# Kernel optimization log

Hardware: AMD Instinct MI355X
Metric: run time of the kernel (lower is better)

Reference implementation:

```python
import jax, jax.numpy as jnp
import numpy as np

IN, H, OUT, FC_H = 8, 128, 4, 64
BN_EPS = 1e-5


def _lstm_cell(x, h, c, Wih, Whh, bih, bhh):
    # PyTorch gate order: i, f, g, o
    z = x @ Wih.T + h @ Whh.T + (bih + bhh)  # [B, 4H]
    i, f, g, o = jnp.split(z, 4, axis=-1)
    i, f, o = jax.nn.sigmoid(i), jax.nn.sigmoid(f), jax.nn.sigmoid(o)
    g = jnp.tanh(g)
    c = f * c + i * g
    h = o * jnp.tanh(c)
    return h, c


def setup_inputs() -> dict:
    key = jax.random.key(0)
    ks = jax.random.split(key, 20)
    s = 0.05
    inp = {
        "x": jax.random.normal(ks[0], (4096, 512, IN), jnp.float32),
        # LSTM layer 0 (input_size -> H)
        "Wih0": jax.random.normal(ks[1], (4 * H, IN), jnp.float32) * s,
        "Whh0": jax.random.normal(ks[2], (4 * H, H), jnp.float32) * s,
        "bih0": jax.random.normal(ks[3], (4 * H,), jnp.float32) * s,
        "bhh0": jax.random.normal(ks[4], (4 * H,), jnp.float32) * s,
        # LSTM layer 1 (H -> H)
        "Wih1": jax.random.normal(ks[5], (4 * H, H), jnp.float32) * s,
        "Whh1": jax.random.normal(ks[6], (4 * H, H), jnp.float32) * s,
        "bih1": jax.random.normal(ks[7], (4 * H,), jnp.float32) * s,
        "bhh1": jax.random.normal(ks[8], (4 * H,), jnp.float32) * s,
        # BatchNorm1d(H) in eval mode: affine params + running stats
        "bn_gamma": jnp.ones((H,), jnp.float32),
        "bn_beta": jnp.zeros((H,), jnp.float32),
        "bn_mean": jax.random.normal(ks[9], (H,), jnp.float32) * s,
        "bn_var": jax.random.uniform(ks[10], (H,), jnp.float32, 0.5, 1.5),
        # fc: Linear(H, 64) -> ReLU -> Linear(64, OUT)
        "W1": jax.random.normal(ks[11], (FC_H, H), jnp.float32) * s,
        "b1": jax.random.normal(ks[12], (FC_H,), jnp.float32) * s,
        "W2": jax.random.normal(ks[13], (OUT, FC_H), jnp.float32) * s,
        "b2": jax.random.normal(ks[14], (OUT,), jnp.float32) * s,
        # feedback: Linear(OUT, IN)
        "Wf": jax.random.normal(ks[15], (IN, OUT), jnp.float32) * s,
        "bf": jax.random.normal(ks[16], (IN,), jnp.float32) * s,
        "prediction_steps": 64,
    }
    return inp


def reference(x, Wih0, Whh0, bih0, bhh0, Wih1, Whh1, bih1, bhh1,
              bn_gamma, bn_beta, bn_mean, bn_var, W1, b1, W2, b2, Wf, bf,
              prediction_steps):
    B = x.shape[0]
    h0 = jnp.zeros((B, H), x.dtype)
    state0 = (h0, h0, h0, h0)  # (h_l0, c_l0, h_l1, c_l1)

    def step(state, xt):
        hl0, cl0, hl1, cl1 = state
        hl0, cl0 = _lstm_cell(xt, hl0, cl0, Wih0, Whh0, bih0, bhh0)
        hl1, cl1 = _lstm_cell(hl0, hl1, cl1, Wih1, Whh1, bih1, bhh1)
        return (hl0, cl0, hl1, cl1), None

    # Encoding pass over the full sequence (seq_len=1 per step in torch loop)
    xs = jnp.swapaxes(x, 0, 1)  # [T, B, IN]
    state, _ = jax.lax.scan(step, state0, xs)

    def fc(h):
        hn = (h - bn_mean) * jax.lax.rsqrt(bn_var + BN_EPS) * bn_gamma + bn_beta
        return jax.nn.relu(hn @ W1.T + b1) @ W2.T + b2

    def dec_step(carry, _):
        hl0, cl0, hl1, cl1, xin = carry
        hl0, cl0 = _lstm_cell(xin, hl0, cl0, Wih0, Whh0, bih0, bhh0)
        hl1, cl1 = _lstm_cell(hl0, hl1, cl1, Wih1, Whh1, bih1, bhh1)
        out = fc(hl1)                 # [B, OUT]
        xin = out @ Wf.T + bf         # feedback -> next input [B, IN]
        return (hl0, cl0, hl1, cl1, xin), out

    carry0 = (*state, x[:, -1, :])
    _, outs = jax.lax.scan(dec_step, carry0, None, length=prediction_steps)
    return jnp.swapaxes(outs, 0, 1)  # [B, prediction_steps, OUT]
```

## Files before the change

### kernel.cpp

```cpp
#include <hip/hip_runtime.h>

#define THREADS 512
#define BT 16
#define TLEN 512
#define HD 128
#define NT 4
#define WSTR 132
#define HSTR 136

#define SC_IFO (-1.4426950408889634f)
#define SC_G   ( 2.8853900817779268f)

typedef __attribute__((ext_vector_type(8))) short bf16x8;
typedef __attribute__((ext_vector_type(4))) float f32x4;

__device__ __forceinline__ short f2bf(float f) {
  unsigned u = __float_as_uint(f);
  u += 0x7fff + ((u >> 16) & 1);
  return (short)(u >> 16);
}

__device__ __forceinline__ unsigned cvt_pk_bf16(float lo, float hi) {
  unsigned r;
  asm("v_cvt_pk_bf16_f32 %0, %1, %2" : "=v"(r) : "v"(lo), "v"(hi));
  return r;
}

__device__ __forceinline__ bf16x8 pack8(f32x4 a, f32x4 b) {
  bf16x8 r;
  r[0]=f2bf(a[0]); r[1]=f2bf(a[1]); r[2]=f2bf(a[2]); r[3]=f2bf(a[3]);
  r[4]=f2bf(b[0]); r[5]=f2bf(b[1]); r[6]=f2bf(b[2]); r[7]=f2bf(b[3]);
  return r;
}
__device__ __forceinline__ bf16x8 load8(const float* p) {
  const f32x4* q4 = (const f32x4*)p;
  return pack8(q4[0], q4[1]);
}
__device__ __forceinline__ bf16x8 load8s(const float* p, float s) {
  const f32x4* q4 = (const f32x4*)p;
  return pack8(q4[0] * s, q4[1] * s);
}

__global__ __launch_bounds__(THREADS, 2) void lstm_kernel(
    const float* __restrict__ xg,
    const float* __restrict__ Wih0, const float* __restrict__ Whh0,
    const float* __restrict__ bih0, const float* __restrict__ bhh0,
    const float* __restrict__ Wih1, const float* __restrict__ Whh1,
    const float* __restrict__ bih1, const float* __restrict__ bhh1,
    const float* __restrict__ gma, const float* __restrict__ bta,
    const float* __restrict__ mu,  const float* __restrict__ var,
    const float* __restrict__ W1,  const float* __restrict__ b1,
    const float* __restrict__ W2,  const float* __restrict__ b2,
    const float* __restrict__ Wf,  const float* __restrict__ bfv,
    const int* __restrict__ psP,
    float* __restrict__ dout)
{
  __shared__ __align__(16) short WhhL[512*WSTR];
  __shared__ __align__(16) short h0A[2][BT*HSTR];
  __shared__ __align__(16) short h1A[2][BT*HSTR];
  __shared__ __align__(16) short xA[2][BT*32];
  __shared__ float a1L[64*BT];
  __shared__ float W2L[4*65];
  __shared__ float outL[4*BT];
  __shared__ float WfL[8*4];
  __shared__ float b2L[4];
  __shared__ float bfL[8];
  __shared__ float b1cL[64];
  __shared__ float sLs[HD];

  const int tid = threadIdx.x;
  const int w   = tid >> 6;
  const int l   = tid & 63;
  const int ln  = l & 15;
  const int q   = l >> 4;
  const int gb0 = blockIdx.x * BT;
  const int ps  = psP[0];

  for (int i = tid; i < BT*32; i += THREADS) { xA[0][i] = 0; xA[1][i] = 0; }
  for (int i = tid; i < BT*HSTR; i += THREADS) {
    h0A[0][i] = 0; h0A[1][i] = 0; h1A[0][i] = 0; h1A[1][i] = 0;
  }
  if (tid < BT) {
    xA[0][tid*32 + 8] = (short)0x3F80;
    xA[1][tid*32 + 8] = (short)0x3F80;
  }
  if (tid < HD) sLs[tid] = gma[tid] * rsqrtf(var[tid] + 1e-5f);
  if (tid < 260) { int o = tid / 65, p = tid % 65; W2L[tid] = (p < 64) ? W2[o*64 + p] : 0.f; }
  if (tid < 32) WfL[tid] = Wf[tid];
  if (tid < 4)  b2L[tid] = b2[tid];
  if (tid < 8)  bfL[tid] = bfv[tid];
  for (int i = tid; i < 512*HD; i += THREADS) {
    int og = i >> 7, k = i & 127;
    float sc = ((og >> 7) == 2) ? SC_G : SC_IFO;
    WhhL[og*WSTR + k] = f2bf(Whh0[i] * sc);
  }

  bf16x8 wih0f[NT], wih1f[NT][4], whh1f[NT][4];
  float b1sum[NT];
  #pragma unroll
  for (int nt = 0; nt < NT; nt++) {
    int og = nt*HD + (w << 4) + ln;
    const float sc = (nt == 2) ? SC_G : SC_IFO;
    {
      bf16x8 r;
      #pragma unroll
      for (int j = 0; j < 8; j++) {
        int k = q*8 + j;
        float v = 0.f;
        if (k < 8) v = Wih0[og*8 + k];
        else if (k == 8) v = bih0[og] + bhh0[og];
        r[j] = f2bf(v * sc);
      }
      wih0f[nt] = r;
    }
    #pragma unroll
    for (int kk = 0; kk < 4; kk++) {
      int k0 = kk*32 + q*8;
      wih1f[nt][kk] = load8s(Wih1 + og*HD + k0, sc);
      whh1f[nt][kk] = load8s(Whh1 + og*HD + k0, sc);
    }
    b1sum[nt] = (bih1[og] + bhh1[og]) * sc;
  }
  __syncthreads();

  if (tid < 64) {
    float acc = b1[tid];
    for (int j = 0; j < HD; j++)
      acc += (bta[j] - mu[j]*sLs[j]) * W1[tid*HD + j];
    b1cL[tid] = acc;
  }
  if (tid < 128) {
    const int b = tid >> 3, i2 = tid & 7;
    xA[0][b*32 + i2] = f2bf(xg[(size_t)(gb0 + b)*(TLEN*8) + i2]);
  }
  __syncthreads();

  f32x4 c0s = {0.f,0.f,0.f,0.f};
  f32x4 c1s = {0.f,0.f,0.f,0.f};

  const int aoffX = ln*32   + q*8;
  const int aoffH = ln*HSTR + q*8;
  const int hwoff = (q*4)*HSTR + (w<<4) + ln;

  auto gates = [&](const f32x4& gi, const f32x4& gf, const f32x4& gg, const f32x4& go,
                   f32x4& cs, short* hw) {
    float hv[4];
    #pragma unroll
    for (int r = 0; r < 4; r++) {
      float ei = __builtin_amdgcn_exp2f(gi[r]);
      float ef = __builtin_amdgcn_exp2f(gf[r]);
      float eg = __builtin_amdgcn_exp2f(gg[r]);
      float eo = __builtin_amdgcn_exp2f(go[r]);
      float f   = __builtin_amdgcn_rcpf(1.0f + ef);
      float rig = __builtin_amdgcn_rcpf((1.0f + ei) * (1.0f + eg));
      float igs = (SC_G * eg - SC_G) * rig;
      float c   = f * cs[r] + igs;
      cs[r] = c;
      float ec  = __builtin_amdgcn_exp2f(c);
      float roc = __builtin_amdgcn_rcpf((1.0f + eo) * (1.0f + ec));
      hv[r] = (ec - 1.0f) * roc;
    }
    unsigned p01 = cvt_pk_bf16(hv[0], hv[1]);
    unsigned p23 = cvt_pk_bf16(hv[2], hv[3]);
    hw[0*HSTR] = (short)p01;
    hw[1*HSTR] = (short)(p01 >> 16);
    hw[2*HSTR] = (short)p23;
    hw[3*HSTR] = (short)(p23 >> 16);
  };

  auto layer0 = [&](const short* xr, const bf16x8* ah, short* h0w) {
    bf16x8 ax = *(const bf16x8*)(xr + aoffX);
    f32x4 ac[NT];
    #pragma unroll
    for (int nt = 0; nt < NT; nt++) {
      const int cb = (nt*HD + (w<<4) + ln)*WSTR + q*8;
      f32x4 a = {0.f,0.f,0.f,0.f};
      a = __builtin_amdgcn_mfma_f32_16x16x32_bf16(ax, wih0f[nt], a, 0, 0, 0);
      #pragma unroll
      for (int kk = 0; kk < 4; kk++) {
        bf16x8 wb = *(const bf16x8*)(WhhL + cb + kk*32);
        a = __builtin_amdgcn_mfma_f32_16x16x32_bf16(ah[kk], wb, a, 0, 0, 0);
      }
      ac[nt] = a;
    }
    gates(ac[0], ac[1], ac[2], ac[3], c0s, h0w + hwoff);
  };

  auto layer1 = [&](const bf16x8* ah, const short* h1r, short* h1w) {
    bf16x8 a1k[4];
    #pragma unroll
    for (int kk = 0; kk < 4; kk++)
      a1k[kk] = *(const bf16x8*)(h1r + aoffH + kk*32);
    f32x4 ac[NT];
    #pragma unroll
    for (int nt = 0; nt < NT; nt++) {
      f32x4 a; a[0]=a[1]=a[2]=a[3]=b1sum[nt];
      #pragma unroll
      for (int kk = 0; kk < 4; kk++) {
        a = __builtin_amdgcn_mfma_f32_16x16x32_bf16(ah[kk],  wih1f[nt][kk], a, 0, 0, 0);
        a = __builtin_amdgcn_mfma_f32_16x16x32_bf16(a1k[kk], whh1f[nt][kk], a, 0, 0, 0);
      }
      ac[nt] = a;
    }
    gates(ac[0], ac[1], ac[2], ac[3], c1s, h1w + hwoff);
  };

  auto enc_iter = [&](int k, const short* xr, short* xw,
                      const short* h0r, short* h0w,
                      const short* h1r, short* h1w, bool doL0, bool doL1) {
    const int b = tid >> 3, i2 = tid & 7;
    const bool pf = doL0 && (k + 1 < TLEN) && (tid < 128);
    float xp = 0.f;
    if (pf) xp = xg[(size_t)(gb0 + b)*(TLEN*8) + (size_t)(k+1)*8 + i2];
    bf16x8 ah[4];
    #pragma unroll
    for (int kk = 0; kk < 4; kk++)
      ah[kk] = *(const bf16x8*)(h0r + aoffH + kk*32);
    if (doL0) layer0(xr, ah, h0w);
    if (doL1) layer1(ah, h1r, h1w);
    if (pf) xw[b*32 + i2] = f2bf(xp);
    __syncthreads();
  };

  enc_iter(0, xA[0], xA[1], h0A[1], h0A[0], h1A[0], h1A[1], true, false);
  enc_iter(1, xA[1], xA[0], h0A[0], h0A[1], h1A[1], h1A[0], true, true);
  for (int k = 2; k < TLEN; k += 2) {
    enc_iter(k,     xA[0], xA[1], h0A[1], h0A[0], h1A[0], h1A[1], true, true);
    enc_iter(k + 1, xA[1], xA[0], h0A[0], h0A[1], h1A[1], h1A[0], true, true);
  }
  enc_iter(TLEN, xA[0], xA[1], h0A[1], h0A[0], h1A[0], h1A[1], false, true);

  bf16x8 w1f[4];
  #pragma unroll
  for (int kk = 0; kk < 4; kk++) {
    bf16x8 r;
    if (w < 4) {
      int p = w*16 + ln;
      #pragma unroll
      for (int j = 0; j < 8; j++) {
        int k = kk*32 + q*8 + j;
        r[j] = f2bf(sLs[k] * W1[p*HD + k]);
      }
    } else {
      #pragma unroll
      for (int j = 0; j < 8; j++) r[j] = 0;
    }
    w1f[kk] = r;
  }

  for (int s = 0; s < ps; s++) {
    int rb = (s & 1) ^ 1;
    __syncthreads();
    {
      bf16x8 ah[4];
      #pragma unroll
      for (int kk = 0; kk < 4; kk++)
        ah[kk] = *(const bf16x8*)(h0A[rb] + aoffH + kk*32);
      layer0(xA[1], ah, h0A[rb^1]);
    }
    __syncthreads();
    {
      bf16x8 ah[4];
      #pragma unroll
      for (int kk = 0; kk < 4; kk++)
        ah[kk] = *(const bf16x8*)(h0A[rb^1] + aoffH + kk*32);
      layer1(ah, h1A[rb], h1A[rb^1]);
    }
    const short* h1n = h1A[rb^1];
    __syncthreads();
    if (w < 4) {
      f32x4 aa = {0.f,0.f,0.f,0.f};
      #pragma unroll
      for (int kk = 0; kk < 4; kk++) {
        bf16x8 ahn = *(const bf16x8*)(h1n + aoffH + kk*32);
        aa = __builtin_amdgcn_mfma_f32_16x16x32_bf16(ahn, w1f[kk], aa, 0, 0, 0);
      }
      float bb = b1cL[w*16 + ln];
      #pragma unroll
      for (int r = 0; r < 4; r++)
        a1L[(w*16 + ln)*16 + q*4 + r] = fmaxf(aa[r] + bb, 0.f);
    }
    __syncthreads();
    if (tid < 64) {
      int b = tid & 15, o = tid >> 4;
      float acc2 = b2L[o];
      for (int p = 0; p < 64; p++)
        acc2 += a1L[p*16 + b] * W2L[o*65 + p];
      dout[(size_t)(gb0 + b)*(ps*4) + s*4 + o] = acc2;
      outL[o*16 + b] = acc2;
    }
    __syncthreads();
    if (tid < 128) {
      int b = tid >> 3, i2 = tid & 7;
      float v = bfL[i2];
      #pragma unroll
      for (int o = 0; o < 4; o++) v += outL[o*16 + b] * WfL[i2*4 + o];
      xA[1][b*32 + i2] = f2bf(v);
    }
  }
}

extern "C" void kernel_launch(void* const* d_in, const int* in_sizes, int n_in,
                              void* d_out, int out_size, void* d_ws, size_t ws_size,
                              hipStream_t stream) {
  (void)in_sizes; (void)n_in; (void)d_ws; (void)ws_size; (void)out_size;
  lstm_kernel<<<dim3(4096/BT), dim3(THREADS), 0, stream>>>(
      (const float*)d_in[0],  (const float*)d_in[1],  (const float*)d_in[2],
      (const float*)d_in[3],  (const float*)d_in[4],  (const float*)d_in[5],
      (const float*)d_in[6],  (const float*)d_in[7],  (const float*)d_in[8],
      (const float*)d_in[9],  (const float*)d_in[10], (const float*)d_in[11],
      (const float*)d_in[12], (const float*)d_in[13], (const float*)d_in[14],
      (const float*)d_in[15], (const float*)d_in[16], (const float*)d_in[17],
      (const float*)d_in[18], (const int*)d_in[19],   (float*)d_out);
}
```

Measured before the change: 1.401 ms.

## Fold feedback into FC2 weights and interleave layer MFMA chains in encoder

Precomputes a combined Wf·W2 matrix and bias so the decoder's next input comes straight from the ReLU activations. This removes one barrier and the serial outL→feedback stage, and the feedback and output dot products now run in parallel on separate thread groups. The encoder step is also inlined so both layers' MFMA chains are issued before either gate computation, which should increase instruction-level overlap. The cost is higher register pressure from holding both accumulators and the h1 operands at once.

```diff
diff --git a/kernel.cpp b/kernel.cpp
--- a/kernel.cpp
+++ b/kernel.cpp
@@ -31,10 +31,6 @@
   r[0]=f2bf(a[0]); r[1]=f2bf(a[1]); r[2]=f2bf(a[2]); r[3]=f2bf(a[3]);
   r[4]=f2bf(b[0]); r[5]=f2bf(b[1]); r[6]=f2bf(b[2]); r[7]=f2bf(b[3]);
   return r;
-}
-__device__ __forceinline__ bf16x8 load8(const float* p) {
-  const f32x4* q4 = (const f32x4*)p;
-  return pack8(q4[0], q4[1]);
 }
 __device__ __forceinline__ bf16x8 load8s(const float* p, float s) {
   const f32x4* q4 = (const f32x4*)p;
@@ -61,10 +57,9 @@
   __shared__ __align__(16) short xA[2][BT*32];
   __shared__ float a1L[64*BT];
   __shared__ float W2L[4*65];
-  __shared__ float outL[4*BT];
-  __shared__ float WfL[8*4];
+  __shared__ float WcL[8*68];
+  __shared__ float bcL[8];
   __shared__ float b2L[4];
-  __shared__ float bfL[8];
   __shared__ float b1cL[64];
   __shared__ float sLs[HD];
 
@@ -86,9 +81,20 @@
   }
   if (tid < HD) sLs[tid] = gma[tid] * rsqrtf(var[tid] + 1e-5f);
   if (tid < 260) { int o = tid / 65, p = tid % 65; W2L[tid] = (p < 64) ? W2[o*64 + p] : 0.f; }
-  if (tid < 32) WfL[tid] = Wf[tid];
+  {
+    int i0 = tid >> 6, p = tid & 63;
+    float acc = 0.f;
+    #pragma unroll
+    for (int o = 0; o < 4; o++) acc += Wf[i0*4 + o] * W2[o*64 + p];
+    WcL[i0*68 + p] = acc;
+  }
+  if (tid < 8) {
+    float acc = bfv[tid];
+    #pragma unroll
+    for (int o = 0; o < 4; o++) acc += Wf[tid*4 + o] * b2[o];
+    bcL[tid] = acc;
+  }
   if (tid < 4)  b2L[tid] = b2[tid];
-  if (tid < 8)  bfL[tid] = bfv[tid];
   for (int i = tid; i < 512*HD; i += THREADS) {
     int og = i >> 7, k = i & 127;
     float sc = ((og >> 7) == 2) ? SC_G : SC_IFO;
@@ -216,8 +222,42 @@
     #pragma unroll
     for (int kk = 0; kk < 4; kk++)
       ah[kk] = *(const bf16x8*)(h0r + aoffH + kk*32);
-    if (doL0) layer0(xr, ah, h0w);
-    if (doL1) layer1(ah, h1r, h1w);
+    bf16x8 a1k[4];
+    if (doL1) {
+      #pragma unroll
+      for (int kk = 0; kk < 4; kk++)
+        a1k[kk] = *(const bf16x8*)(h1r + aoffH + kk*32);
+    }
+    f32x4 ac0[NT], ac1[NT];
+    if (doL0) {
+      bf16x8 ax = *(const bf16x8*)(xr + aoffX);
+      #pragma unroll
+      for (int nt = 0; nt < NT; nt++) {
+        const int cb = (nt*HD + (w<<4) + ln)*WSTR + q*8;
+        f32x4 a = {0.f,0.f,0.f,0.f};
+        a = __builtin_amdgcn_mfma_f32_16x16x32_bf16(ax, wih0f[nt], a, 0, 0, 0);
+        #pragma unroll
+        for (int kk = 0; kk < 4; kk++) {
+          bf16x8 wb = *(const bf16x8*)(WhhL + cb + kk*32);
+          a = __builtin_amdgcn_mfma_f32_16x16x32_bf16(ah[kk], wb, a, 0, 0, 0);
+        }
+        ac0[nt] = a;
+      }
+    }
+    if (doL1) {
+      #pragma unroll
+      for (int nt = 0; nt < NT; nt++) {
+        f32x4 a; a[0]=a[1]=a[2]=a[3]=b1sum[nt];
+        #pragma unroll
+        for (int kk = 0; kk < 4; kk++) {
+          a = __builtin_amdgcn_mfma_f32_16x16x32_bf16(ah[kk],  wih1f[nt][kk], a, 0, 0, 0);
+          a = __builtin_amdgcn_mfma_f32_16x16x32_bf16(a1k[kk], whh1f[nt][kk], a, 0, 0, 0);
+        }
+        ac1[nt] = a;
+      }
+    }
+    if (doL0) gates(ac0[0], ac0[1], ac0[2], ac0[3], c0s, h0w + hwoff);
+    if (doL1) gates(ac1[0], ac1[1], ac1[2], ac1[3], c1s, h1w + hwoff);
     if (pf) xw[b*32 + i2] = f2bf(xp);
     __syncthreads();
   };
@@ -281,21 +321,18 @@
         a1L[(w*16 + ln)*16 + q*4 + r] = fmaxf(aa[r] + bb, 0.f);
     }
     __syncthreads();
-    if (tid < 64) {
-      int b = tid & 15, o = tid >> 4;
+    if (tid < 128) {
+      int b = tid >> 3, i2 = tid & 7;
+      float v = bcL[i2];
+      for (int p = 0; p < 64; p++)
+        v += a1L[p*16 + b] * WcL[i2*68 + p];
+      xA[1][b*32 + i2] = f2bf(v);
+    } else if (tid < 192) {
+      int t = tid - 128, b = t & 15, o = t >> 4;
       float acc2 = b2L[o];
       for (int p = 0; p < 64; p++)
         acc2 += a1L[p*16 + b] * W2L[o*65 + p];
       dout[(size_t)(gb0 + b)*(ps*4) + s*4 + o] = acc2;
-      outL[o*16 + b] = acc2;
-    }
-    __syncthreads();
-    if (tid < 128) {
-      int b = tid >> 3, i2 = tid & 7;
-      float v = bfL[i2];
-      #pragma unroll
-      for (int o = 0; o < 4; o++) v += outL[o*16 + b] * WfL[i2*4 + o];
-      xA[1][b*32 + i2] = f2bf(v);
     }
   }
 }
```

After: 1.266 ms. 9.6% less time.
